# Optimization experiments

Hardware: AMD Instinct MI355X
Metric: run time of the kernel (lower is better)

## Reference

```python
import jax, jax.numpy as jnp
import numpy as np

B, H, W = 4, 256, 256
DIM = 180
NH = 6
WH, WW = 16, 16          # window size
BH, BW = 8, 8            # base window size
CH = DIM // (2 * NH)     # per-head dim = 15
SCALE = float(CH)        # note: divide by head_dim (not sqrt), as in source
RH, RW = WH // BH, WW // BW
R = RH * RW              # spatial reduction ratio = 4
L = WH * WW              # 256 tokens per window
BL = BH * BW             # 64 base tokens
POS_DIM = (DIM // 4) // 4  # 11


def _rel_index(Hs, Ws):
    coords = np.stack(np.meshgrid(np.arange(Hs), np.arange(Ws), indexing='ij')).reshape(2, -1)
    rel = (coords[:, :, None] - coords[:, None, :]).transpose(1, 2, 0)
    rel[..., 0] += Hs - 1
    rel[..., 1] += Ws - 1
    rel[..., 0] *= 2 * Ws - 1
    return rel.sum(-1)  # (L, L) int

RPI = _rel_index(WH, WW)


def _ln(x, g, b):
    mu = x.mean(-1, keepdims=True)
    var = ((x - mu) ** 2).mean(-1, keepdims=True)
    return (x - mu) / jnp.sqrt(var + 1e-5) * g + b


def _conv(x, w, b):  # x: NHWC, w: HWIO
    y = jax.lax.conv_general_dilated(x, w, (1, 1), 'SAME',
                                     dimension_numbers=('NHWC', 'HWIO', 'NHWC'))
    return y + b


def setup_inputs():
    key = jax.random.key(0)
    ks = jax.random.split(key, 12)
    def wgt(k, shape, s=0.05):
        return jax.random.normal(k, shape, jnp.float32) * s
    C5 = DIM // 5
    d = {}
    d['x'] = jax.random.normal(ks[0], (B, H, W, DIM), jnp.float32)
    d['dfe_c1_w'] = wgt(ks[1], (1, 1, DIM, C5)); d['dfe_c1_b'] = jnp.zeros((C5,), jnp.float32)
    d['dfe_c2_w'] = wgt(ks[2], (3, 3, C5, C5));  d['dfe_c2_b'] = jnp.zeros((C5,), jnp.float32)
    d['dfe_c3_w'] = wgt(ks[3], (1, 1, C5, DIM)); d['dfe_c3_b'] = jnp.zeros((DIM,), jnp.float32)
    d['dfe_lin_w'] = wgt(ks[4], (1, 1, DIM, DIM)); d['dfe_lin_b'] = jnp.zeros((DIM,), jnp.float32)
    d['sl_w'] = wgt(ks[5], (1, R), 0.5); d['sl_b'] = jnp.zeros((1,), jnp.float32)
    d['pos_proj_w'] = wgt(ks[6], (POS_DIM, 2), 0.1); d['pos_proj_b'] = jnp.zeros((POS_DIM,), jnp.float32)
    for i, kk in zip((1, 2), (ks[7], ks[8])):
        d['pos%d_ln_g' % i] = jnp.ones((POS_DIM,), jnp.float32)
        d['pos%d_ln_b' % i] = jnp.zeros((POS_DIM,), jnp.float32)
        d['pos%d_w' % i] = wgt(kk, (POS_DIM, POS_DIM), 0.1)
        d['pos%d_b' % i] = jnp.zeros((POS_DIM,), jnp.float32)
    d['pos3_ln_g'] = jnp.ones((POS_DIM,), jnp.float32)
    d['pos3_ln_b'] = jnp.zeros((POS_DIM,), jnp.float32)
    d['pos3_w'] = wgt(ks[9], (NH, POS_DIM), 0.1)
    d['pos3_b'] = jnp.zeros((NH,), jnp.float32)
    d['proj_w'] = wgt(ks[10], (DIM, DIM))
    d['proj_b'] = jnp.zeros((DIM,), jnp.float32)
    return d


def reference(x, dfe_c1_w, dfe_c1_b, dfe_c2_w, dfe_c2_b, dfe_c3_w, dfe_c3_b,
              dfe_lin_w, dfe_lin_b, sl_w, sl_b, pos_proj_w, pos_proj_b,
              pos1_ln_g, pos1_ln_b, pos1_w, pos1_b,
              pos2_ln_g, pos2_ln_b, pos2_w, pos2_b,
              pos3_ln_g, pos3_ln_b, pos3_w, pos3_b,
              proj_w, proj_b):
    Bb, Hh, Ww_, C = x.shape
    # ---- DFE: qv = conv_path(x) * linear_path(x) ----
    t = jax.nn.leaky_relu(_conv(x, dfe_c1_w, dfe_c1_b), 0.2)
    t = jax.nn.leaky_relu(_conv(t, dfe_c2_w, dfe_c2_b), 0.2)
    t = _conv(t, dfe_c3_w, dfe_c3_b)
    qv = t * _conv(x, dfe_lin_w, dfe_lin_b)  # (B,H,W,C)
    # ---- window partition ----
    qv = qv.reshape(Bb, Hh // WH, WH, Ww_ // WW, WW, C).transpose(0, 1, 3, 2, 4, 5)
    qv = qv.reshape(-1, L, C)                       # (B_, L, C)
    B_ = qv.shape[0]
    qv = qv.reshape(B_, L, 2, NH, CH)
    q = qv[:, :, 0].transpose(0, 2, 1, 3)           # (B_, NH, L, CH)
    v = qv[:, :, 1].transpose(0, 2, 1, 3)           # (B_, NH, L, CH)
    # ---- spatial linear projection of v to base window ----
    vp = v.reshape(B_, NH, BH, RH, BW, RW, CH).transpose(0, 1, 2, 4, 6, 3, 5)
    vp = vp.reshape(B_, NH, BL, CH, R)
    vp = jnp.einsum('bnlcr,r->bnlc', vp, sl_w[0]) + sl_b[0]  # (B_, NH, BL, CH)
    # ---- spatial self-correlation ----
    corr = jnp.einsum('bnlc,bnmc->bnlm', q, vp) / SCALE       # (B_, NH, L, BL)
    # dynamic relative position bias (non-residual MLP)
    ph = jnp.arange(1 - WH, WH)
    pw = jnp.arange(1 - WW, WW)
    biases = jnp.stack(jnp.meshgrid(ph, pw, indexing='ij')).reshape(2, -1).T.astype(x.dtype)
    p = biases @ pos_proj_w.T + pos_proj_b
    p = jax.nn.relu(_ln(p, pos1_ln_g, pos1_ln_b)) @ pos1_w.T + pos1_b
    p = jax.nn.relu(_ln(p, pos2_ln_g, pos2_ln_b)) @ pos2_w.T + pos2_b
    pos = jax.nn.relu(_ln(p, pos3_ln_g, pos3_ln_b)) @ pos3_w.T + pos3_b  # ((2WH-1)(2WW-1), NH)
    rpb = pos[RPI.reshape(-1)].reshape(L, L, NH).transpose(2, 0, 1)      # (NH, L, L)
    rpb = rpb.reshape(NH, L, BH, RH, BW, RW).transpose(0, 1, 2, 4, 3, 5)
    rpb = rpb.reshape(NH, L, BL, R).mean(-1)                             # (NH, L, BL)
    corr = corr + rpb[None]
    x_sp = jnp.einsum('bnlm,bnmc->bnlc', corr, vp)
    x_sp = x_sp.transpose(0, 2, 1, 3).reshape(B_, L, C // 2)
    # ---- channel self-correlation (single-head) ----
    qc = q.transpose(0, 2, 1, 3).reshape(B_, L, C // 2)
    vc = v.transpose(0, 2, 1, 3).reshape(B_, L, C // 2)
    cmap = jnp.einsum('blc,bld->bcd', qc, vc) / float(L)                 # (B_, C/2, C/2)
    x_ch = jnp.einsum('bcd,bld->blc', cmap, vc)                          # (B_, L, C/2)
    # ---- window reverse + fuse ----
    def rev(a):
        c = a.shape[-1]
        a = a.reshape(Bb, Hh // WH, Ww_ // WW, WH, WW, c).transpose(0, 1, 3, 2, 4, 5)
        return a.reshape(Bb, Hh, Ww_, c)
    x_sp = rev(x_sp.reshape(B_, WH, WW, C // 2))
    x_ch = rev(x_ch.reshape(B_, WH, WW, C // 2))
    out = jnp.concatenate([x_sp, x_ch], -1) @ proj_w.T + proj_b          # (B,H,W,C)
    return out
```

## Files before the change

### kernel.cpp

```cpp
#include <hip/hip_runtime.h>

#define LEAKY(v) ((v) > 0.f ? (v) : 0.2f * (v))

__device__ __forceinline__ void ln_relu11(float* p, const float* __restrict__ g,
                                          const float* __restrict__ b) {
  float mu = 0.f;
#pragma unroll
  for (int j = 0; j < 11; ++j) mu += p[j];
  mu *= (1.f / 11.f);
  float var = 0.f;
#pragma unroll
  for (int j = 0; j < 11; ++j) { float d = p[j] - mu; var += d * d; }
  var *= (1.f / 11.f);
  float inv = 1.f / sqrtf(var + 1e-5f);
#pragma unroll
  for (int j = 0; j < 11; ++j) {
    float v = (p[j] - mu) * inv * g[j] + b[j];
    p[j] = v > 0.f ? v : 0.f;
  }
}

__global__ void pos_mlp_kernel(
    const float* __restrict__ w0, const float* __restrict__ b0,
    const float* __restrict__ g1, const float* __restrict__ be1,
    const float* __restrict__ w1, const float* __restrict__ b1,
    const float* __restrict__ g2, const float* __restrict__ be2,
    const float* __restrict__ w2, const float* __restrict__ b2,
    const float* __restrict__ g3, const float* __restrict__ be3,
    const float* __restrict__ w3, const float* __restrict__ b3,
    float* __restrict__ pos_out) {
  int r = blockIdx.x * 256 + threadIdx.x;
  if (r >= 961) return;
  float bh = (float)(r / 31 - 15);
  float bw = (float)(r % 31 - 15);
  float p[11], q[11];
#pragma unroll
  for (int j = 0; j < 11; ++j) p[j] = bh * w0[2 * j] + bw * w0[2 * j + 1] + b0[j];
  ln_relu11(p, g1, be1);
#pragma unroll
  for (int j = 0; j < 11; ++j) {
    float s = b1[j];
#pragma unroll
    for (int k = 0; k < 11; ++k) s += p[k] * w1[j * 11 + k];
    q[j] = s;
  }
  ln_relu11(q, g2, be2);
#pragma unroll
  for (int j = 0; j < 11; ++j) {
    float s = b2[j];
#pragma unroll
    for (int k = 0; k < 11; ++k) s += q[k] * w2[j * 11 + k];
    p[j] = s;
  }
  ln_relu11(p, g3, be3);
#pragma unroll
  for (int n = 0; n < 6; ++n) {
    float s = b3[n];
#pragma unroll
    for (int k = 0; k < 11; ++k) s += p[k] * w3[n * 11 + k];
    pos_out[r * 6 + n] = s;
  }
}

__global__ void rpb_kernel(const float* __restrict__ pos, float* __restrict__ rpb) {
  int o = blockIdx.x * 256 + threadIdx.x;
  int n = o >> 14;
  int l = (o >> 6) & 255;
  int m = o & 63;
  int i1 = l >> 4, j1 = l & 15;
  int bi = m >> 3, bj = m & 7;
  float s = 0.f;
#pragma unroll
  for (int rh = 0; rh < 2; ++rh)
#pragma unroll
    for (int rw = 0; rw < 2; ++rw) {
      int i2 = bi * 2 + rh, j2 = bj * 2 + rw;
      int idx = (i1 - i2 + 15) * 31 + (j1 - j2 + 15);
      s += pos[idx * 6 + n];
    }
  rpb[o] = s * 0.25f;
}

__global__ void pt_kernel(const float* __restrict__ pjw, float* __restrict__ pt) {
  int i = blockIdx.x * 256 + threadIdx.x;
  if (i >= 180 * 180) return;
  int c = i / 180, k = i % 180;
  pt[c * 180 + k] = pjw[k * 180 + c];
}

__global__ __launch_bounds__(256) void dfe1_kernel(const float* __restrict__ x,
                                                   const float* __restrict__ w1,
                                                   const float* __restrict__ b1,
                                                   float* __restrict__ t1) {
  __shared__ float xt[256][36];
  int t = threadIdx.x;
  int p0 = blockIdx.x * 256;
  float acc[36];
#pragma unroll
  for (int j = 0; j < 36; ++j) acc[j] = 0.f;
  for (int kc = 0; kc < 5; ++kc) {
    __syncthreads();
    for (int idx = t; idx < 256 * 36; idx += 256) {
      int px = idx / 36, ci = idx % 36;
      xt[px][ci] = x[(p0 + px) * 180 + kc * 36 + ci];
    }
    __syncthreads();
    for (int ci = 0; ci < 36; ++ci) {
      float v = xt[t][ci];
      const float* wr = &w1[(kc * 36 + ci) * 36];
#pragma unroll
      for (int j = 0; j < 36; ++j) acc[j] += v * wr[j];
    }
  }
  float* o = &t1[(p0 + t) * 36];
#pragma unroll
  for (int j = 0; j < 36; ++j) {
    float v = acc[j] + b1[j];
    o[j] = LEAKY(v);
  }
}

__global__ __launch_bounds__(256) void dfe2_kernel(const float* __restrict__ t1,
                                                   const float* __restrict__ w2,
                                                   const float* __restrict__ b2,
                                                   float* __restrict__ t2) {
  __shared__ float halo[18][18][36];
  int t = threadIdx.x;
  int blk = blockIdx.x;
  int img = blk >> 8;
  int rem = blk & 255;
  int ty0 = (rem >> 4) << 4;
  int tx0 = (rem & 15) << 4;
  for (int idx = t; idx < 18 * 18 * 36; idx += 256) {
    int ci = idx % 36;
    int xx = (idx / 36) % 18;
    int yy = idx / (36 * 18);
    int gy = ty0 + yy - 1;
    int gx = tx0 + xx - 1;
    float v = 0.f;
    if (gy >= 0 && gy < 256 && gx >= 0 && gx < 256)
      v = t1[((img * 256 + gy) * 256 + gx) * 36 + ci];
    halo[yy][xx][ci] = v;
  }
  __syncthreads();
  int ly = t >> 4, lx = t & 15;
  float acc[36];
#pragma unroll
  for (int j = 0; j < 36; ++j) acc[j] = 0.f;
#pragma unroll
  for (int kh = 0; kh < 3; ++kh)
#pragma unroll
    for (int kw = 0; kw < 3; ++kw) {
      for (int ci = 0; ci < 36; ++ci) {
        float v = halo[ly + kh][lx + kw][ci];
        const float* wr = &w2[((kh * 3 + kw) * 36 + ci) * 36];
#pragma unroll
        for (int j = 0; j < 36; ++j) acc[j] += v * wr[j];
      }
    }
  float* o = &t2[((img * 256 + ty0 + ly) * 256 + tx0 + lx) * 36];
#pragma unroll
  for (int j = 0; j < 36; ++j) {
    float v = acc[j] + b2[j];
    o[j] = LEAKY(v);
  }
}

__global__ __launch_bounds__(256, 2) void dfe3_kernel(const float* __restrict__ x,
                                                      const float* __restrict__ t2,
                                                      const float* __restrict__ w3,
                                                      const float* __restrict__ b3,
                                                      const float* __restrict__ wl,
                                                      const float* __restrict__ bl,
                                                      float* __restrict__ qv) {
  __shared__ __align__(16) float As[36 * 132];
  __shared__ __align__(16) float Bs[36 * 180 + 16];
  int t = threadIdx.x;
  int tx = t & 15;
  int ty = t >> 4;
  int p0 = blockIdx.x * 128;

  int pA0 = t / 9,           cA0 = t - pA0 * 9;
  int pA1 = (t + 256) / 9,   cA1 = (t + 256) - pA1 * 9;
  int pA2 = (t + 512) / 9,   cA2 = (t + 512) - pA2 * 9;
  int pA3 = (t + 768) / 9,   cA3 = (t + 768) - pA3 * 9;
  int pA4 = (t + 1024) / 9,  cA4 = (t + 1024) - pA4 * 9;
  const float4* xf4  = (const float4*)x;
  const float4* t2f4 = (const float4*)t2;
  const float4* wlf4 = (const float4*)wl;
  const float4* w3f4 = (const float4*)w3;
  float4* Bs4 = (float4*)Bs;

  float4 a0, a1, a2, a3, a4;
  float4 bF0, bF1, bF2, bF3, bF4, bF5, bF6;
  a4 = make_float4(0.f, 0.f, 0.f, 0.f);
  bF6 = make_float4(0.f, 0.f, 0.f, 0.f);

  auto scatterA = [&](int pa, int ca, float4 v) {
    As[(ca * 4 + 0) * 132 + pa] = v.x;
    As[(ca * 4 + 1) * 132 + pa] = v.y;
    As[(ca * 4 + 2) * 132 + pa] = v.z;
    As[(ca * 4 + 3) * 132 + pa] = v.w;
  };
  auto stage_write = [&]() {
    scatterA(pA0, cA0, a0);
    scatterA(pA1, cA1, a1);
    scatterA(pA2, cA2, a2);
    scatterA(pA3, cA3, a3);
    if (t < 128) scatterA(pA4, cA4, a4);
    Bs4[t] = bF0;
    Bs4[t + 256] = bF1;
    Bs4[t + 512] = bF2;
    Bs4[t + 768] = bF3;
    Bs4[t + 1024] = bF4;
    Bs4[t + 1280] = bF5;
    if (t < 84) Bs4[t + 1536] = bF6;
  };

  auto issue_lin = [&](int kc) {
    int kb = kc * 9;
    a0 = xf4[(size_t)(p0 + pA0) * 45 + kb + cA0];
    a1 = xf4[(size_t)(p0 + pA1) * 45 + kb + cA1];
    a2 = xf4[(size_t)(p0 + pA2) * 45 + kb + cA2];
    a3 = xf4[(size_t)(p0 + pA3) * 45 + kb + cA3];
    if (t < 128) a4 = xf4[(size_t)(p0 + pA4) * 45 + kb + cA4];
    int kw = kc * 1620;
    bF0 = wlf4[kw + t];
    bF1 = wlf4[kw + t + 256];
    bF2 = wlf4[kw + t + 512];
    bF3 = wlf4[kw + t + 768];
    bF4 = wlf4[kw + t + 1024];
    bF5 = wlf4[kw + t + 1280];
    if (t < 84) bF6 = wlf4[kw + t + 1536];
  };
  auto issue_conv = [&]() {
    a0 = t2f4[(size_t)(p0 + pA0) * 9 + cA0];
    a1 = t2f4[(size_t)(p0 + pA1) * 9 + cA1];
    a2 = t2f4[(size_t)(p0 + pA2) * 9 + cA2];
    a3 = t2f4[(size_t)(p0 + pA3) * 9 + cA3];
    if (t < 128) a4 = t2f4[(size_t)(p0 + pA4) * 9 + cA4];
    bF0 = w3f4[t];
    bF1 = w3f4[t + 256];
    bF2 = w3f4[t + 512];
    bF3 = w3f4[t + 768];
    bF4 = w3f4[t + 1024];
    bF5 = w3f4[t + 1280];
    if (t < 84) bF6 = w3f4[t + 1536];
  };

  auto compute36 = [&](float acc[8][12]) {
    for (int ci = 0; ci < 36; ++ci) {
      const float4* ap = (const float4*)&As[ci * 132 + ty * 8];
      float4 A0 = ap[0], A1 = ap[1];
      const float* bp = &Bs[ci * 180 + tx * 12];
      float4 B0 = *(const float4*)bp;
      float4 B1 = *(const float4*)(bp + 4);
      float4 B2 = *(const float4*)(bp + 8);
      float av[8] = {A0.x, A0.y, A0.z, A0.w, A1.x, A1.y, A1.z, A1.w};
      float bv[12] = {B0.x, B0.y, B0.z, B0.w, B1.x, B1.y, B1.z, B1.w,
                      B2.x, B2.y, B2.z, B2.w};
#pragma unroll
      for (int r = 0; r < 8; ++r)
#pragma unroll
        for (int j = 0; j < 12; ++j) acc[r][j] += av[r] * bv[j];
    }
  };

  issue_lin(0);
  float accL[8][12];
#pragma unroll
  for (int r = 0; r < 8; ++r)
#pragma unroll
    for (int j = 0; j < 12; ++j) accL[r][j] = 0.f;

#pragma unroll 1
  for (int p = 0; p < 5; ++p) {
    stage_write();
    __syncthreads();
    if (p < 4) issue_lin(p + 1); else issue_conv();
    compute36(accL);
    __syncthreads();
  }

  if (tx < 15) {
#pragma unroll
    for (int r = 0; r < 8; ++r) {
      int base = (p0 + ty * 8 + r) * 180 + tx * 12;
#pragma unroll
      for (int j = 0; j < 12; ++j) qv[base + j] = accL[r][j] + bl[tx * 12 + j];
    }
  }

  float accC[8][12];
#pragma unroll
  for (int r = 0; r < 8; ++r)
#pragma unroll
    for (int j = 0; j < 12; ++j) accC[r][j] = 0.f;
  stage_write();
  __syncthreads();
  compute36(accC);

  if (tx < 15) {
#pragma unroll
    for (int r = 0; r < 8; ++r) {
      int base = (p0 + ty * 8 + r) * 180 + tx * 12;
#pragma unroll
      for (int j = 0; j < 12; ++j) {
        float lp = qv[base + j];
        qv[base + j] = (accC[r][j] + b3[tx * 12 + j]) * lp;
      }
    }
  }
}

__global__ __launch_bounds__(256, 4) void att_sp_kernel(
    const float* __restrict__ qv, const float* __restrict__ slw,
    const float* __restrict__ slb, const float* __restrict__ rpb,
    const float* __restrict__ pt, const float* __restrict__ pb,
    float* __restrict__ out) {
  __shared__ __align__(16) float vp[6][64][16];
  __shared__ float xsp[128][91];
  int t = threadIdx.x;
  int wb = blockIdx.x;
  int b = wb >> 8, wi = (wb >> 4) & 15, wj = wb & 15;
  int wbase = (b * 256 + wi * 16) * 256 + wj * 16;
  float wsl0 = slw[0], wsl1 = slw[1], wsl2 = slw[2], wsl3 = slw[3];
  float bsl = slb[0];

  for (int idx = t; idx < 6 * 64 * 16; idx += 256) {
    int n = idx >> 10;
    int m = (idx >> 4) & 63;
    int ch = idx & 15;
    float s = 0.f;
    if (ch < 15) {
      int bi = m >> 3, bj = m & 7;
      int pa00 = (wbase + (bi * 2) * 256 + bj * 2) * 180 + 90 + n * 15 + ch;
      s = qv[pa00] * wsl0;
      s += qv[pa00 + 180] * wsl1;
      s += qv[pa00 + 256 * 180] * wsl2;
      s += qv[pa00 + 257 * 180] * wsl3;
      s += bsl;
    }
    vp[n][m][ch] = s;
  }
  __syncthreads();

  int lt = t & 127;
  int hg = t >> 7;
  const float inv15 = 1.f / 15.f;

#pragma unroll 1
  for (int half = 0; half < 2; ++half) {
    int l = half * 128 + lt;
    int pa = (wbase + (l >> 4) * 256 + (l & 15)) * 180;
#pragma unroll 1
    for (int nn = 0; nn < 3; ++nn) {
      int n = hg * 3 + nn;
      float qh[15];
#pragma unroll
      for (int c = 0; c < 15; ++c) qh[c] = qv[pa + n * 15 + c];
      float xs[15];
#pragma unroll
      for (int c = 0; c < 15; ++c) xs[c] = 0.f;
      const float* rp = &rpb[(n * 256 + l) * 64];
#pragma unroll 4
      for (int m4 = 0; m4 < 16; ++m4) {
        float4 rpv = *(const float4*)(rp + m4 * 4);
        float rparr[4] = {rpv.x, rpv.y, rpv.z, rpv.w};
#pragma unroll
        for (int mm = 0; mm < 4; ++mm) {
          const float4* vr = (const float4*)(&vp[n][m4 * 4 + mm][0]);
          float4 v0 = vr[0], v1 = vr[1], v2 = vr[2], v3 = vr[3];
          float d0 = qh[0] * v0.x + qh[1] * v0.y;
          float d1 = qh[2] * v0.z + qh[3] * v0.w;
          float d2 = qh[4] * v1.x + qh[5] * v1.y;
          float d3 = qh[6] * v1.z + qh[7] * v1.w;
          float d4 = qh[8] * v2.x + qh[9] * v2.y;
          float d5 = qh[10] * v2.z + qh[11] * v2.w;
          float d6 = qh[12] * v3.x + qh[13] * v3.y;
          float d7 = qh[14] * v3.z;
          float e0 = d0 + d1, e1 = d2 + d3, e2 = d4 + d5, e3 = d6 + d7;
          float s = (e0 + e1) + (e2 + e3);
          s = s * inv15 + rparr[mm];
          xs[0] += s * v0.x; xs[1] += s * v0.y; xs[2] += s * v0.z; xs[3] += s * v0.w;
          xs[4] += s * v1.x; xs[5] += s * v1.y; xs[6] += s * v1.z; xs[7] += s * v1.w;
          xs[8] += s * v2.x; xs[9] += s * v2.y; xs[10] += s * v2.z; xs[11] += s * v2.w;
          xs[12] += s * v3.x; xs[13] += s * v3.y; xs[14] += s * v3.z;
        }
      }
#pragma unroll
      for (int c = 0; c < 15; ++c) xsp[lt][n * 15 + c] = xs[c];
    }
    __syncthreads();
    {
      int lane = t & 63;
      int w4 = __builtin_amdgcn_readfirstlane(t >> 6);
      int k0 = w4 * 45;
      const float* ptb = pt + k0;
#pragma unroll 1
      for (int tok2 = 0; tok2 < 2; ++tok2) {
        int tt = tok2 * 64 + lane;
        int l2 = half * 128 + tt;
        int pa2 = (wbase + (l2 >> 4) * 256 + (l2 & 15)) * 180 + k0;
        float pacc[45];
#pragma unroll
        for (int j = 0; j < 45; ++j) pacc[j] = pb[k0 + j];
#pragma unroll 2
        for (int c = 0; c < 90; ++c) {
          float xv = xsp[tt][c];
          const float* prw = ptb + c * 180;
#pragma unroll
          for (int j = 0; j < 45; ++j) pacc[j] += xv * prw[j];
        }
        float* op = out + pa2;
#pragma unroll
        for (int j = 0; j < 45; ++j) op[j] = pacc[j];
      }
    }
    __syncthreads();
  }
}

__global__ __launch_bounds__(256, 2) void cmapM_kernel(const float* __restrict__ qv,
                                                       const float* __restrict__ p2t,
                                                       float* __restrict__ M) {
  __shared__ float cmt[90][91];
  __shared__ float bufA[32][97];
  __shared__ float vtt[32][97];
  int t = threadIdx.x;
  int wb = blockIdx.x;
  int b = wb >> 8, wi = (wb >> 4) & 15, wj = wb & 15;
  int wbase = (b * 256 + wi * 16) * 256 + wj * 16;

  int tx = t & 15, ty = t >> 4;
  float acc[6][6];
#pragma unroll
  for (int i = 0; i < 6; ++i)
#pragma unroll
    for (int j = 0; j < 6; ++j) acc[i][j] = 0.f;

#pragma unroll 1
  for (int ck = 0; ck < 8; ++ck) {
    __syncthreads();
    for (int idx = t; idx < 32 * 97; idx += 256) {
      int l = idx / 97, c = idx % 97;
      int gl = ck * 32 + l;
      int pa = (wbase + (gl >> 4) * 256 + (gl & 15)) * 180;
      bufA[l][c] = (c < 90) ? qv[pa + c] : 0.f;
      vtt[l][c] = (c < 90) ? qv[pa + 90 + c] : 0.f;
    }
    __syncthreads();
    for (int lk = 0; lk < 32; ++lk) {
      float aa[6], bb[6];
#pragma unroll
      for (int i = 0; i < 6; ++i) aa[i] = bufA[lk][tx * 6 + i];
#pragma unroll
      for (int j = 0; j < 6; ++j) bb[j] = vtt[lk][ty * 6 + j];
#pragma unroll
      for (int i = 0; i < 6; ++i)
#pragma unroll
        for (int j = 0; j < 6; ++j) acc[i][j] += aa[i] * bb[j];
    }
  }
  __syncthreads();
  if (tx < 15 && ty < 15) {
#pragma unroll
    for (int i = 0; i < 6; ++i)
#pragma unroll
      for (int j = 0; j < 6; ++j) cmt[tx * 6 + i][ty * 6 + j] = acc[i][j] * (1.f / 256.f);
  }
  __syncthreads();

  int lane = t & 63;
  int kq = __builtin_amdgcn_readfirstlane(t >> 6);
  int k0 = kq * 45;
  int d0 = lane;
  int d1 = lane + 64;
  int d1c = (d1 < 90) ? d1 : 0;
  float m0[45], m1[45];
#pragma unroll
  for (int j = 0; j < 45; ++j) { m0[j] = 0.f; m1[j] = 0.f; }
#pragma unroll 1
  for (int c = 0; c < 90; ++c) {
    const float* pr = p2t + c * 180 + k0;
    float v0 = cmt[c][d0];
    float v1 = cmt[c][d1c];
#pragma unroll
    for (int j = 0; j < 45; ++j) {
      float p = pr[j];
      m0[j] += p * v0;
      m1[j] += p * v1;
    }
  }
  float* M0 = M + (size_t)wb * 16200 + d0 * 180 + k0;
#pragma unroll
  for (int j = 0; j < 45; ++j) M0[j] = m0[j];
  if (d1 < 90) {
    float* M1 = M + (size_t)wb * 16200 + d1 * 180 + k0;
#pragma unroll
    for (int j = 0; j < 45; ++j) M1[j] = m1[j];
  }
}

__global__ __launch_bounds__(256, 4) void chupd_kernel(const float* __restrict__ qv,
                                                       const float* __restrict__ M,
                                                       float* __restrict__ out) {
  __shared__ float vt[64][91];
  int bid = blockIdx.x;
  int wb = bid >> 2, grp = bid & 3;
  int b = wb >> 8, wi = (wb >> 4) & 15, wj = wb & 15;
  int wbase = (b * 256 + wi * 16) * 256 + wj * 16;
  int t = threadIdx.x;

  for (int idx = t; idx < 64 * 90; idx += 256) {
    int l = idx / 90, d = idx - l * 90;
    int gl = grp * 64 + l;
    int pa = (wbase + (gl >> 4) * 256 + (gl & 15)) * 180;
    vt[l][d] = qv[pa + 90 + d];
  }
  __syncthreads();

  int l = t & 63;
  int kq = __builtin_amdgcn_readfirstlane(t >> 6);
  int k0 = kq * 45;
  const float* Mw = M + (size_t)wb * 16200;
  float pacc[45];
#pragma unroll
  for (int j = 0; j < 45; ++j) pacc[j] = 0.f;
#pragma unroll 2
  for (int d = 0; d < 90; ++d) {
    const float* mr = Mw + d * 180 + k0;
    float vl = vt[l][d];
#pragma unroll
    for (int j = 0; j < 45; ++j) pacc[j] += mr[j] * vl;
  }
  int gl = grp * 64 + l;
  int pa = (wbase + (gl >> 4) * 256 + (gl & 15)) * 180 + k0;
#pragma unroll
  for (int j = 0; j < 45; ++j) out[pa + j] += pacc[j];
}

extern "C" void kernel_launch(void* const* d_in, const int* in_sizes, int n_in,
                              void* d_out, int out_size, void* d_ws, size_t ws_size,
                              hipStream_t stream) {
  (void)in_sizes; (void)n_in; (void)out_size; (void)ws_size;
  const float* x   = (const float*)d_in[0];
  const float* w1  = (const float*)d_in[1];
  const float* b1  = (const float*)d_in[2];
  const float* w2  = (const float*)d_in[3];
  const float* b2  = (const float*)d_in[4];
  const float* w3  = (const float*)d_in[5];
  const float* b3  = (const float*)d_in[6];
  const float* wl  = (const float*)d_in[7];
  const float* bl  = (const float*)d_in[8];
  const float* slw = (const float*)d_in[9];
  const float* slb = (const float*)d_in[10];
  const float* pw0 = (const float*)d_in[11];
  const float* pb0 = (const float*)d_in[12];
  const float* g1  = (const float*)d_in[13];
  const float* be1 = (const float*)d_in[14];
  const float* mw1 = (const float*)d_in[15];
  const float* mb1 = (const float*)d_in[16];
  const float* g2  = (const float*)d_in[17];
  const float* be2 = (const float*)d_in[18];
  const float* mw2 = (const float*)d_in[19];
  const float* mb2 = (const float*)d_in[20];
  const float* g3  = (const float*)d_in[21];
  const float* be3 = (const float*)d_in[22];
  const float* mw3 = (const float*)d_in[23];
  const float* mb3 = (const float*)d_in[24];
  const float* pjw = (const float*)d_in[25];
  const float* pjb = (const float*)d_in[26];
  float* out = (float*)d_out;
  float* ws  = (float*)d_ws;

  float* qv  = ws;
  float* t1  = ws + 47185920;
  float* t2  = t1 + 9437184;
  float* pos = t2 + 9437184;
  float* rpb = pos + 5768;
  float* M   = t1;
  float* pt  = t1 + 18874368 - 32768;

  pos_mlp_kernel<<<4, 256, 0, stream>>>(pw0, pb0, g1, be1, mw1, mb1,
                                        g2, be2, mw2, mb2, g3, be3, mw3, mb3, pos);
  rpb_kernel<<<384, 256, 0, stream>>>(pos, rpb);
  dfe1_kernel<<<1024, 256, 0, stream>>>(x, w1, b1, t1);
  dfe2_kernel<<<1024, 256, 0, stream>>>(t1, w2, b2, t2);
  dfe3_kernel<<<2048, 256, 0, stream>>>(x, t2, w3, b3, wl, bl, qv);
  pt_kernel<<<127, 256, 0, stream>>>(pjw, pt);
  att_sp_kernel<<<1024, 256, 0, stream>>>(qv, slw, slb, rpb, pt, pjb, out);
  cmapM_kernel<<<1024, 256, 0, stream>>>(qv, pt + 90 * 180, M);
  chupd_kernel<<<4096, 256, 0, stream>>>(qv, M, out);
}
```

Measured before the change: 1.346 ms.

## Fuse channel-branch update into spatial attention projection epilogue

Runs the cmapM kernel before att_sp and folds the chupd matmul (v times the per-window M matrix) into att_sp's output projection loop, accumulating into the same registers before the single store. This removes one kernel launch and the read-modify-write pass over the output tensor, along with the separate staging of v. In exchange, att_sp now reads M and v straight from global memory inside its inner loop, which lengthens that kernel and could raise register pressure.

After: 1.489 ms. 1.11x slower.

```diff
diff --git a/kernel.cpp b/kernel.cpp
--- a/kernel.cpp
+++ b/kernel.cpp
@@ -313,11 +313,92 @@
   }
 }
 
+__global__ __launch_bounds__(256, 2) void cmapM_kernel(const float* __restrict__ qv,
+                                                       const float* __restrict__ p2t,
+                                                       float* __restrict__ M) {
+  __shared__ float cmt[90][91];
+  __shared__ float bufA[32][97];
+  __shared__ float vtt[32][97];
+  int t = threadIdx.x;
+  int wb = blockIdx.x;
+  int b = wb >> 8, wi = (wb >> 4) & 15, wj = wb & 15;
+  int wbase = (b * 256 + wi * 16) * 256 + wj * 16;
+
+  int tx = t & 15, ty = t >> 4;
+  float acc[6][6];
+#pragma unroll
+  for (int i = 0; i < 6; ++i)
+#pragma unroll
+    for (int j = 0; j < 6; ++j) acc[i][j] = 0.f;
+
+#pragma unroll 1
+  for (int ck = 0; ck < 8; ++ck) {
+    __syncthreads();
+    for (int idx = t; idx < 32 * 97; idx += 256) {
+      int l = idx / 97, c = idx % 97;
+      int gl = ck * 32 + l;
+      int pa = (wbase + (gl >> 4) * 256 + (gl & 15)) * 180;
+      bufA[l][c] = (c < 90) ? qv[pa + c] : 0.f;
+      vtt[l][c] = (c < 90) ? qv[pa + 90 + c] : 0.f;
+    }
+    __syncthreads();
+    for (int lk = 0; lk < 32; ++lk) {
+      float aa[6], bb[6];
+#pragma unroll
+      for (int i = 0; i < 6; ++i) aa[i] = bufA[lk][tx * 6 + i];
+#pragma unroll
+      for (int j = 0; j < 6; ++j) bb[j] = vtt[lk][ty * 6 + j];
+#pragma unroll
+      for (int i = 0; i < 6; ++i)
+#pragma unroll
+        for (int j = 0; j < 6; ++j) acc[i][j] += aa[i] * bb[j];
+    }
+  }
+  __syncthreads();
+  if (tx < 15 && ty < 15) {
+#pragma unroll
+    for (int i = 0; i < 6; ++i)
+#pragma unroll
+      for (int j = 0; j < 6; ++j) cmt[tx * 6 + i][ty * 6 + j] = acc[i][j] * (1.f / 256.f);
+  }
+  __syncthreads();
+
+  int lane = t & 63;
+  int kq = __builtin_amdgcn_readfirstlane(t >> 6);
+  int k0 = kq * 45;
+  int d0 = lane;
+  int d1 = lane + 64;
+  int d1c = (d1 < 90) ? d1 : 0;
+  float m0[45], m1[45];
+#pragma unroll
+  for (int j = 0; j < 45; ++j) { m0[j] = 0.f; m1[j] = 0.f; }
+#pragma unroll 1
+  for (int c = 0; c < 90; ++c) {
+    const float* pr = p2t + c * 180 + k0;
+    float v0 = cmt[c][d0];
+    float v1 = cmt[c][d1c];
+#pragma unroll
+    for (int j = 0; j < 45; ++j) {
+      float p = pr[j];
+      m0[j] += p * v0;
+      m1[j] += p * v1;
+    }
+  }
+  float* M0 = M + (size_t)wb * 16200 + d0 * 180 + k0;
+#pragma unroll
+  for (int j = 0; j < 45; ++j) M0[j] = m0[j];
+  if (d1 < 90) {
+    float* M1 = M + (size_t)wb * 16200 + d1 * 180 + k0;
+#pragma unroll
+    for (int j = 0; j < 45; ++j) M1[j] = m1[j];
+  }
+}
+
 __global__ __launch_bounds__(256, 4) void att_sp_kernel(
     const float* __restrict__ qv, const float* __restrict__ slw,
     const float* __restrict__ slb, const float* __restrict__ rpb,
     const float* __restrict__ pt, const float* __restrict__ pb,
-    float* __restrict__ out) {
+    const float* __restrict__ M, float* __restrict__ out) {
   __shared__ __align__(16) float vp[6][64][16];
   __shared__ float xsp[128][91];
   int t = threadIdx.x;
@@ -348,6 +429,7 @@
   int lt = t & 127;
   int hg = t >> 7;
   const float inv15 = 1.f / 15.f;
+  const float* Mw = M + (size_t)wb * 16200;
 
 #pragma unroll 1
   for (int half = 0; half < 2; ++half) {
@@ -397,11 +479,12 @@
       int w4 = __builtin_amdgcn_readfirstlane(t >> 6);
       int k0 = w4 * 45;
       const float* ptb = pt + k0;
+      const float* Mb = Mw + k0;
 #pragma unroll 1
       for (int tok2 = 0; tok2 < 2; ++tok2) {
         int tt = tok2 * 64 + lane;
         int l2 = half * 128 + tt;
-        int pa2 = (wbase + (l2 >> 4) * 256 + (l2 & 15)) * 180 + k0;
+        int pbase = (wbase + (l2 >> 4) * 256 + (l2 & 15)) * 180;
         float pacc[45];
 #pragma unroll
         for (int j = 0; j < 45; ++j) pacc[j] = pb[k0 + j];
@@ -412,132 +495,24 @@
 #pragma unroll
           for (int j = 0; j < 45; ++j) pacc[j] += xv * prw[j];
         }
-        float* op = out + pa2;
+        const float* vb = qv + pbase + 90;
+#pragma unroll 2
+        for (int d = 0; d < 90; d += 2) {
+          float2 vv = *(const float2*)(vb + d);
+          const float* mr0 = Mb + d * 180;
+          const float* mr1 = mr0 + 180;
+#pragma unroll
+          for (int j = 0; j < 45; ++j) pacc[j] += vv.x * mr0[j];
+#pragma unroll
+          for (int j = 0; j < 45; ++j) pacc[j] += vv.y * mr1[j];
+        }
+        float* op = out + pbase + k0;
 #pragma unroll
         for (int j = 0; j < 45; ++j) op[j] = pacc[j];
       }
     }
     __syncthreads();
   }
-}
-
-__global__ __launch_bounds__(256, 2) void cmapM_kernel(const float* __restrict__ qv,
-                                                       const float* __restrict__ p2t,
-                                                       float* __restrict__ M) {
-  __shared__ float cmt[90][91];
-  __shared__ float bufA[32][97];
-  __shared__ float vtt[32][97];
-  int t = threadIdx.x;
-  int wb = blockIdx.x;
-  int b = wb >> 8, wi = (wb >> 4) & 15, wj = wb & 15;
-  int wbase = (b * 256 + wi * 16) * 256 + wj * 16;
-
-  int tx = t & 15, ty = t >> 4;
-  float acc[6][6];
-#pragma unroll
-  for (int i = 0; i < 6; ++i)
-#pragma unroll
-    for (int j = 0; j < 6; ++j) acc[i][j] = 0.f;
-
-#pragma unroll 1
-  for (int ck = 0; ck < 8; ++ck) {
-    __syncthreads();
-    for (int idx = t; idx < 32 * 97; idx += 256) {
-      int l = idx / 97, c = idx % 97;
-      int gl = ck * 32 + l;
-      int pa = (wbase + (gl >> 4) * 256 + (gl & 15)) * 180;
-      bufA[l][c] = (c < 90) ? qv[pa + c] : 0.f;
-      vtt[l][c] = (c < 90) ? qv[pa + 90 + c] : 0.f;
-    }
-    __syncthreads();
-    for (int lk = 0; lk < 32; ++lk) {
-      float aa[6], bb[6];
-#pragma unroll
-      for (int i = 0; i < 6; ++i) aa[i] = bufA[lk][tx * 6 + i];
-#pragma unroll
-      for (int j = 0; j < 6; ++j) bb[j] = vtt[lk][ty * 6 + j];
-#pragma unroll
-      for (int i = 0; i < 6; ++i)
-#pragma unroll
-        for (int j = 0; j < 6; ++j) acc[i][j] += aa[i] * bb[j];
-    }
-  }
-  __syncthreads();
-  if (tx < 15 && ty < 15) {
-#pragma unroll
-    for (int i = 0; i < 6; ++i)
-#pragma unroll
-      for (int j = 0; j < 6; ++j) cmt[tx * 6 + i][ty * 6 + j] = acc[i][j] * (1.f / 256.f);
-  }
-  __syncthreads();
-
-  int lane = t & 63;
-  int kq = __builtin_amdgcn_readfirstlane(t >> 6);
-  int k0 = kq * 45;
-  int d0 = lane;
-  int d1 = lane + 64;
-  int d1c = (d1 < 90) ? d1 : 0;
-  float m0[45], m1[45];
-#pragma unroll
-  for (int j = 0; j < 45; ++j) { m0[j] = 0.f; m1[j] = 0.f; }
-#pragma unroll 1
-  for (int c = 0; c < 90; ++c) {
-    const float* pr = p2t + c * 180 + k0;
-    float v0 = cmt[c][d0];
-    float v1 = cmt[c][d1c];
-#pragma unroll
-    for (int j = 0; j < 45; ++j) {
-      float p = pr[j];
-      m0[j] += p * v0;
-      m1[j] += p * v1;
-    }
-  }
-  float* M0 = M + (size_t)wb * 16200 + d0 * 180 + k0;
-#pragma unroll
-  for (int j = 0; j < 45; ++j) M0[j] = m0[j];
-  if (d1 < 90) {
-    float* M1 = M + (size_t)wb * 16200 + d1 * 180 + k0;
-#pragma unroll
-    for (int j = 0; j < 45; ++j) M1[j] = m1[j];
-  }
-}
-
-__global__ __launch_bounds__(256, 4) void chupd_kernel(const float* __restrict__ qv,
-                                                       const float* __restrict__ M,
-                                                       float* __restrict__ out) {
-  __shared__ float vt[64][91];
-  int bid = blockIdx.x;
-  int wb = bid >> 2, grp = bid & 3;
-  int b = wb >> 8, wi = (wb >> 4) & 15, wj = wb & 15;
-  int wbase = (b * 256 + wi * 16) * 256 + wj * 16;
-  int t = threadIdx.x;
-
-  for (int idx = t; idx < 64 * 90; idx += 256) {
-    int l = idx / 90, d = idx - l * 90;
-    int gl = grp * 64 + l;
-    int pa = (wbase + (gl >> 4) * 256 + (gl & 15)) * 180;
-    vt[l][d] = qv[pa + 90 + d];
-  }
-  __syncthreads();
-
-  int l = t & 63;
-  int kq = __builtin_amdgcn_readfirstlane(t >> 6);
-  int k0 = kq * 45;
-  const float* Mw = M + (size_t)wb * 16200;
-  float pacc[45];
-#pragma unroll
-  for (int j = 0; j < 45; ++j) pacc[j] = 0.f;
-#pragma unroll 2
-  for (int d = 0; d < 90; ++d) {
-    const float* mr = Mw + d * 180 + k0;
-    float vl = vt[l][d];
-#pragma unroll
-    for (int j = 0; j < 45; ++j) pacc[j] += mr[j] * vl;
-  }
-  int gl = grp * 64 + l;
-  int pa = (wbase + (gl >> 4) * 256 + (gl & 15)) * 180 + k0;
-#pragma unroll
-  for (int j = 0; j < 45; ++j) out[pa + j] += pacc[j];
 }
 
 extern "C" void kernel_launch(void* const* d_in, const int* in_sizes, int n_in,
@@ -589,7 +564,6 @@
   dfe2_kernel<<<1024, 256, 0, stream>>>(t1, w2, b2, t2);
   dfe3_kernel<<<2048, 256, 0, stream>>>(x, t2, w3, b3, wl, bl, qv);
   pt_kernel<<<127, 256, 0, stream>>>(pjw, pt);
-  att_sp_kernel<<<1024, 256, 0, stream>>>(qv, slw, slb, rpb, pt, pjb, out);
   cmapM_kernel<<<1024, 256, 0, stream>>>(qv, pt + 90 * 180, M);
-  chupd_kernel<<<4096, 256, 0, stream>>>(qv, M, out);
-}
+  att_sp_kernel<<<1024, 256, 0, stream>>>(qv, slw, slb, rpb, pt, pjb, M, out);
+}
```

## Reassociate spatial attention via per-head Gram matrix of pooled values

Applied to the files above, without the earlier changes.

The linear (softmax-free) spatial correlation term q·vpᵀ·vp is reassociated as q·(vpᵀvp). A per-window, per-head 15x15 Gram matrix is built once in shared memory, and each token then applies it directly. Only the relative-position-bias term still loops over the 64 pooled tokens. This removes the per-token 64x15 dot-product work, at the cost of an extra shared buffer, a sync, and a small Gram stage run by 90 threads, with slightly different floating-point rounding.

Measured after the change: 1.338 ms. No clear change (-0.6%).

```diff
diff --git a/kernel.cpp b/kernel.cpp
--- a/kernel.cpp
+++ b/kernel.cpp
@@ -320,6 +320,7 @@
     float* __restrict__ out) {
   __shared__ __align__(16) float vp[6][64][16];
   __shared__ float xsp[128][91];
+  __shared__ __align__(16) float G[6][15][16];
   int t = threadIdx.x;
   int wb = blockIdx.x;
   int b = wb >> 8, wi = (wb >> 4) & 15, wj = wb & 15;
@@ -345,6 +346,27 @@
   }
   __syncthreads();
 
+  if (t < 90) {
+    int n = t / 15, i = t - n * 15;
+    float acc[15];
+#pragma unroll
+    for (int j = 0; j < 15; ++j) acc[j] = 0.f;
+#pragma unroll 4
+    for (int m = 0; m < 64; ++m) {
+      float vi = vp[n][m][i];
+      const float4* vr = (const float4*)(&vp[n][m][0]);
+      float4 v0 = vr[0], v1 = vr[1], v2 = vr[2], v3 = vr[3];
+      acc[0] += vi * v0.x; acc[1] += vi * v0.y; acc[2] += vi * v0.z; acc[3] += vi * v0.w;
+      acc[4] += vi * v1.x; acc[5] += vi * v1.y; acc[6] += vi * v1.z; acc[7] += vi * v1.w;
+      acc[8] += vi * v2.x; acc[9] += vi * v2.y; acc[10] += vi * v2.z; acc[11] += vi * v2.w;
+      acc[12] += vi * v3.x; acc[13] += vi * v3.y; acc[14] += vi * v3.z;
+    }
+#pragma unroll
+    for (int j = 0; j < 15; ++j) G[n][i][j] = acc[j];
+    G[n][i][15] = 0.f;
+  }
+  __syncthreads();
+
   int lt = t & 127;
   int hg = t >> 7;
   const float inv15 = 1.f / 15.f;
@@ -358,10 +380,20 @@
       int n = hg * 3 + nn;
       float qh[15];
 #pragma unroll
-      for (int c = 0; c < 15; ++c) qh[c] = qv[pa + n * 15 + c];
+      for (int c = 0; c < 15; ++c) qh[c] = qv[pa + n * 15 + c] * inv15;
       float xs[15];
 #pragma unroll
       for (int c = 0; c < 15; ++c) xs[c] = 0.f;
+#pragma unroll 3
+      for (int d = 0; d < 15; ++d) {
+        float qd = qh[d];
+        const float4* gr = (const float4*)(&G[n][d][0]);
+        float4 g0 = gr[0], g1 = gr[1], g2 = gr[2], g3 = gr[3];
+        xs[0] += qd * g0.x; xs[1] += qd * g0.y; xs[2] += qd * g0.z; xs[3] += qd * g0.w;
+        xs[4] += qd * g1.x; xs[5] += qd * g1.y; xs[6] += qd * g1.z; xs[7] += qd * g1.w;
+        xs[8] += qd * g2.x; xs[9] += qd * g2.y; xs[10] += qd * g2.z; xs[11] += qd * g2.w;
+        xs[12] += qd * g3.x; xs[13] += qd * g3.y; xs[14] += qd * g3.z;
+      }
       const float* rp = &rpb[(n * 256 + l) * 64];
 #pragma unroll 4
       for (int m4 = 0; m4 < 16; ++m4) {
@@ -371,17 +403,7 @@
         for (int mm = 0; mm < 4; ++mm) {
           const float4* vr = (const float4*)(&vp[n][m4 * 4 + mm][0]);
           float4 v0 = vr[0], v1 = vr[1], v2 = vr[2], v3 = vr[3];
-          float d0 = qh[0] * v0.x + qh[1] * v0.y;
-          float d1 = qh[2] * v0.z + qh[3] * v0.w;
-          float d2 = qh[4] * v1.x + qh[5] * v1.y;
-          float d3 = qh[6] * v1.z + qh[7] * v1.w;
-          float d4 = qh[8] * v2.x + qh[9] * v2.y;
-          float d5 = qh[10] * v2.z + qh[11] * v2.w;
-          float d6 = qh[12] * v3.x + qh[13] * v3.y;
-          float d7 = qh[14] * v3.z;
-          float e0 = d0 + d1, e1 = d2 + d3, e2 = d4 + d5, e3 = d6 + d7;
-          float s = (e0 + e1) + (e2 + e3);
-          s = s * inv15 + rparr[mm];
+          float s = rparr[mm];
           xs[0] += s * v0.x; xs[1] += s * v0.y; xs[2] += s * v0.z; xs[3] += s * v0.w;
           xs[4] += s * v1.x; xs[5] += s * v1.y; xs[6] += s * v1.z; xs[7] += s * v1.w;
           xs[8] += s * v2.x; xs[9] += s * v2.y; xs[10] += s * v2.z; xs[11] += s * v2.w;
```
